# Optimization experiments

Measured on AMD Instinct MI355X. Metric: run time of the kernel, lower is better.

Reference implementation:

```python
import jax, jax.numpy as jnp
import numpy as np

DIM = 256
HEADS = 8
K_RATIO = 0.25


def setup_inputs() -> dict:
    key = jax.random.key(0)
    ks = jax.random.split(key, 5)
    B, C, S = 4, DIM, 2048
    x = jax.random.normal(ks[0], (B, C, S), dtype=jnp.float32)
    # Conv1d(dim, 3*dim, 1, bias=False) weight -> (3*dim, dim)
    W_qkv = jax.random.normal(ks[1], (3 * DIM, DIM), dtype=jnp.float32) * (1.0 / np.sqrt(DIM))
    # depthwise Conv1d(3*dim, 3*dim, 3, groups=3*dim) weight -> (3*dim, 1, 3)
    W_dw = jax.random.normal(ks[2], (3 * DIM, 1, 3), dtype=jnp.float32) * (1.0 / np.sqrt(3))
    # Conv1d(dim, dim, 1, bias=False) weight -> (dim, dim)
    W_proj = jax.random.normal(ks[3], (DIM, DIM), dtype=jnp.float32) * (1.0 / np.sqrt(DIM))
    temperature = jnp.ones((HEADS, 1, 1), dtype=jnp.float32)
    return {"x": x, "W_qkv": W_qkv, "W_dw": W_dw, "W_proj": W_proj,
            "temperature": temperature}


def _l2norm(t, eps=1e-12):
    # F.normalize: x / max(||x||_2, eps)
    n = jnp.sqrt(jnp.sum(t * t, axis=-1, keepdims=True))
    return t / jnp.maximum(n, eps)


def reference(x, W_qkv, W_dw, W_proj, temperature):
    B, C, S = x.shape
    H = temperature.shape[0]
    hd = C // H
    # 1x1 conv == channel matmul
    qkv = jnp.einsum('oc,bcs->bos', W_qkv, x)  # [B, 3C, S]
    # depthwise conv, kernel 3, pad 1
    qkv = jax.lax.conv_general_dilated(
        qkv, W_dw, window_strides=(1,), padding=[(1, 1)],
        dimension_numbers=('NCH', 'OIH', 'NCH'),
        feature_group_count=3 * C)
    q, k, v = jnp.split(qkv, 3, axis=1)  # each [B, C, S]

    def to_heads(t):
        return t.reshape(B, H, hd, S).transpose(0, 1, 3, 2)  # [B, H, S, hd]

    q = _l2norm(to_heads(q))
    k = _l2norm(to_heads(k))
    v = to_heads(v)

    scores = jnp.einsum('bhsc,bhtc->bhst', q, k) * temperature  # [B,H,S,S]

    topk = max(1, min(S, int(np.ceil(K_RATIO * S))))
    vals, idx = jax.lax.top_k(scores, topk)  # [B,H,S,topk]

    # scatter top-k values into a -inf tensor along the last axis
    N = B * H * S
    sparse = jnp.full((N, S), -jnp.inf, dtype=scores.dtype)
    rows = jnp.arange(N)[:, None]
    sparse = sparse.at[rows, idx.reshape(N, topk)].set(vals.reshape(N, topk))
    sparse = jnp.clip(sparse.reshape(B, H, S, S), -10000.0, 10000.0)

    attn = jax.nn.softmax(sparse, axis=-1)  # dropout p=0.0 -> identity
    out = jnp.einsum('bhst,bhtc->bhsc', attn, v)  # [B,H,S,hd]
    out = out.transpose(0, 1, 3, 2).reshape(B, C, S)  # b (head c) s
    return jnp.einsum('oc,bcs->bos', W_proj, out)
```

## Files before the change

### kernel.cpp

```cpp
#include <hip/hip_runtime.h>
#include <math.h>

typedef __attribute__((ext_vector_type(8))) short short8;
typedef __attribute__((ext_vector_type(4))) float f32x4;
typedef __attribute__((ext_vector_type(2))) unsigned int uint2v;

#define DEV __device__ __forceinline__

static constexpr int B_ = 4, C_ = 256, S_ = 2048, H_ = 8, O3_ = 768;
static constexpr int TOPK = 512;
static constexpr int QT = 16;
static constexpr int HCOLS = 1024;
static constexpr int HSTR = 1028;
static constexpr int PSTH = 1024;
static constexpr size_t K3_LDS_BYTES = (size_t)QT * HSTR * 4;

DEV unsigned cvt_pk_bf16(float a, float b) {
  unsigned r;
  asm("v_cvt_pk_bf16_f32 %0, %1, %2" : "=v"(r) : "v"(a), "v"(b));
  return r;
}
DEV unsigned short f2bf1(float f) { return (unsigned short)(cvt_pk_bf16(f, f) & 0xFFFFu); }
DEV float bf2f(unsigned short h) { return __uint_as_float(((unsigned)h) << 16); }
DEV void hilo(float f, unsigned short& h, unsigned short& l) {
  unsigned p = cvt_pk_bf16(f, f);
  h = (unsigned short)p;
  float r = f - __uint_as_float(p << 16);
  l = (unsigned short)(cvt_pk_bf16(r, r) & 0xFFFFu);
}

__global__ void k_convw(const float* __restrict__ wqkv, const float* __restrict__ wproj,
                        unsigned short* __restrict__ wq_hi, unsigned short* __restrict__ wq_lo,
                        unsigned short* __restrict__ wproj_bf) {
  int i = blockIdx.x * 256 + threadIdx.x;
  if (i < O3_ * C_) {
    unsigned short h, l;
    hilo(wqkv[i], h, l);
    wq_hi[i] = h;
    wq_lo[i] = l;
  }
  if (i < C_ * C_) wproj_bf[i] = f2bf1(wproj[i]);
}

__global__ void k_xt(const float* __restrict__ x, unsigned short* __restrict__ xT_hi,
                     unsigned short* __restrict__ xT_lo) {
  __shared__ float t[32][33];
  int b = blockIdx.z;
  int c0 = blockIdx.y * 32, s0 = blockIdx.x * 32;
  int tx = threadIdx.x, ty = threadIdx.y;
  const float* xb = x + (size_t)b * C_ * S_;
#pragma unroll
  for (int j = 0; j < 4; ++j)
    t[ty + 8 * j][tx] = xb[(size_t)(c0 + ty + 8 * j) * S_ + s0 + tx];
  __syncthreads();
  unsigned short* hb = xT_hi + (size_t)b * S_ * C_;
  unsigned short* lb = xT_lo + (size_t)b * S_ * C_;
#pragma unroll
  for (int j = 0; j < 4; ++j) {
    unsigned short h, l;
    hilo(t[tx][ty + 8 * j], h, l);
    size_t o = (size_t)(s0 + ty + 8 * j) * C_ + c0 + tx;
    hb[o] = h;
    lb[o] = l;
  }
}

__global__ __launch_bounds__(256) void k_qkv(const unsigned short* __restrict__ w_hi,
                                             const unsigned short* __restrict__ w_lo,
                                             const unsigned short* __restrict__ x_hi,
                                             const unsigned short* __restrict__ x_lo,
                                             float* __restrict__ raw) {
  int b = blockIdx.z;
  int m0 = blockIdx.y * 64, n0 = blockIdx.x * 64;
  int tid = threadIdx.x, lane = tid & 63, wid = tid >> 6;
  int l15 = lane & 15, lh = lane >> 4;
  int wm = (wid >> 1) * 32, wn = (wid & 1) * 32;
  const unsigned short* xhb = x_hi + (size_t)b * S_ * C_;
  const unsigned short* xlb = x_lo + (size_t)b * S_ * C_;
  f32x4 acc[2][2] = {};
  int mA = m0 + wm + l15;
  int nB = n0 + wn + l15;
  for (int k0 = 0; k0 < C_; k0 += 32) {
    int kk = k0 + lh * 8;
    short8 a0h = *(const short8*)(w_hi + (size_t)mA * C_ + kk);
    short8 a1h = *(const short8*)(w_hi + (size_t)(mA + 16) * C_ + kk);
    short8 a0l = *(const short8*)(w_lo + (size_t)mA * C_ + kk);
    short8 a1l = *(const short8*)(w_lo + (size_t)(mA + 16) * C_ + kk);
    short8 b0h = *(const short8*)(xhb + (size_t)nB * C_ + kk);
    short8 b1h = *(const short8*)(xhb + (size_t)(nB + 16) * C_ + kk);
    short8 b0l = *(const short8*)(xlb + (size_t)nB * C_ + kk);
    short8 b1l = *(const short8*)(xlb + (size_t)(nB + 16) * C_ + kk);
    acc[0][0] = __builtin_amdgcn_mfma_f32_16x16x32_bf16(a0h, b0h, acc[0][0], 0, 0, 0);
    acc[0][1] = __builtin_amdgcn_mfma_f32_16x16x32_bf16(a0h, b1h, acc[0][1], 0, 0, 0);
    acc[1][0] = __builtin_amdgcn_mfma_f32_16x16x32_bf16(a1h, b0h, acc[1][0], 0, 0, 0);
    acc[1][1] = __builtin_amdgcn_mfma_f32_16x16x32_bf16(a1h, b1h, acc[1][1], 0, 0, 0);
    acc[0][0] = __builtin_amdgcn_mfma_f32_16x16x32_bf16(a0h, b0l, acc[0][0], 0, 0, 0);
    acc[0][1] = __builtin_amdgcn_mfma_f32_16x16x32_bf16(a0h, b1l, acc[0][1], 0, 0, 0);
    acc[1][0] = __builtin_amdgcn_mfma_f32_16x16x32_bf16(a1h, b0l, acc[1][0], 0, 0, 0);
    acc[1][1] = __builtin_amdgcn_mfma_f32_16x16x32_bf16(a1h, b1l, acc[1][1], 0, 0, 0);
    acc[0][0] = __builtin_amdgcn_mfma_f32_16x16x32_bf16(a0l, b0h, acc[0][0], 0, 0, 0);
    acc[0][1] = __builtin_amdgcn_mfma_f32_16x16x32_bf16(a0l, b1h, acc[0][1], 0, 0, 0);
    acc[1][0] = __builtin_amdgcn_mfma_f32_16x16x32_bf16(a1l, b0h, acc[1][0], 0, 0, 0);
    acc[1][1] = __builtin_amdgcn_mfma_f32_16x16x32_bf16(a1l, b1h, acc[1][1], 0, 0, 0);
  }
  float* rawb = raw + (size_t)b * O3_ * S_;
#pragma unroll
  for (int i = 0; i < 2; ++i)
#pragma unroll
    for (int j = 0; j < 2; ++j)
#pragma unroll
      for (int r = 0; r < 4; ++r) {
        int row = m0 + wm + i * 16 + lh * 4 + r;
        int col = n0 + wn + j * 16 + l15;
        rawb[(size_t)row * S_ + col] = acc[i][j][r];
      }
}

DEV float conv3(const float* __restrict__ rp, const float* __restrict__ w, int s) {
  float a = (s > 0) ? rp[s - 1] : 0.f;
  float b = rp[s];
  float c = (s < S_ - 1) ? rp[s + 1] : 0.f;
  return w[0] * a + w[1] * b + w[2] * c;
}

__global__ __launch_bounds__(256) void k_dwnorm(const float* __restrict__ raw,
                                                const float* __restrict__ wdw,
                                                const float* __restrict__ temp,
                                                unsigned short* __restrict__ q_hi,
                                                unsigned short* __restrict__ q_lo,
                                                unsigned short* __restrict__ k_hi,
                                                unsigned short* __restrict__ k_lo,
                                                unsigned short* __restrict__ vt) {
  int b = blockIdx.z, h = blockIdx.y;
  int tid = threadIdx.x;
  int wave = tid >> 6, lane = tid & 63;
  int dg = lane & 7;
  int sl = lane >> 3;
  int s = blockIdx.x * 32 + wave * 8 + sl;
  const float* rawb = raw + (size_t)b * O3_ * S_;
  float tph = temp[h];
  size_t bh = (size_t)(b * H_ + h);
  float qv[4], kv[4], vv[4];
  float sq = 0.f, sk = 0.f;
#pragma unroll
  for (int dd = 0; dd < 4; ++dd) {
    int d = dg * 4 + dd;
    int oq = h * 32 + d;
    float q = conv3(rawb + (size_t)oq * S_, wdw + oq * 3, s);
    qv[dd] = q; sq += q * q;
    int ok = oq + 256;
    float k = conv3(rawb + (size_t)ok * S_, wdw + ok * 3, s);
    kv[dd] = k; sk += k * k;
    int ov = oq + 512;
    vv[dd] = conv3(rawb + (size_t)ov * S_, wdw + ov * 3, s);
  }
#pragma unroll
  for (int m = 1; m < 8; m <<= 1) {
    sq += __shfl_xor(sq, m);
    sk += __shfl_xor(sk, m);
  }
  float iq = tph / fmaxf(sqrtf(sq), 1e-12f);
  float ik = 1.f / fmaxf(sqrtf(sk), 1e-12f);
  size_t base = (bh * S_ + s) * 32 + dg * 4;

  float q0 = qv[0] * iq, q1 = qv[1] * iq, q2 = qv[2] * iq, q3 = qv[3] * iq;
  unsigned qh01 = cvt_pk_bf16(q0, q1), qh23 = cvt_pk_bf16(q2, q3);
  *(uint2v*)(q_hi + base) = uint2v{qh01, qh23};
  float ql0 = q0 - __uint_as_float(qh01 << 16);
  float ql1 = q1 - __uint_as_float(qh01 & 0xFFFF0000u);
  float ql2 = q2 - __uint_as_float(qh23 << 16);
  float ql3 = q3 - __uint_as_float(qh23 & 0xFFFF0000u);
  *(uint2v*)(q_lo + base) = uint2v{cvt_pk_bf16(ql0, ql1), cvt_pk_bf16(ql2, ql3)};

  float k0 = kv[0] * ik, k1 = kv[1] * ik, k2 = kv[2] * ik, k3 = kv[3] * ik;
  unsigned kh01 = cvt_pk_bf16(k0, k1), kh23 = cvt_pk_bf16(k2, k3);
  *(uint2v*)(k_hi + base) = uint2v{kh01, kh23};
  float kl0 = k0 - __uint_as_float(kh01 << 16);
  float kl1 = k1 - __uint_as_float(kh01 & 0xFFFF0000u);
  float kl2 = k2 - __uint_as_float(kh23 << 16);
  float kl3 = k3 - __uint_as_float(kh23 & 0xFFFF0000u);
  *(uint2v*)(k_lo + base) = uint2v{cvt_pk_bf16(kl0, kl1), cvt_pk_bf16(kl2, kl3)};

#pragma unroll
  for (int dd = 0; dd < 4; ++dd) {
    int d = dg * 4 + dd;
    vt[(bh * 32 + d) * S_ + s] = f2bf1(vv[dd]);
  }
}

__global__ __launch_bounds__(1024, 8) void k_attn(const unsigned short* __restrict__ q_hi,
                                                  const unsigned short* __restrict__ q_lo,
                                                  const unsigned short* __restrict__ k_hi,
                                                  const unsigned short* __restrict__ k_lo,
                                                  const unsigned short* __restrict__ vt,
                                                  unsigned short* __restrict__ ao) {
  extern __shared__ float smem[];
  __shared__ float is_arr[QT];
  float* sc = smem;
  unsigned short* P = (unsigned short*)smem;
  float* red = smem;
  int bid = blockIdx.x;
  int tile = bid & 127;
  int bh = bid >> 7;
  int q0 = tile * QT;
  int tid = threadIdx.x, lane = tid & 63, wv = tid >> 6;
  int l15 = lane & 15, lh = lane >> 4;
  const unsigned short* vb = vt + (size_t)bh * 32 * S_;

  size_t qoff = ((size_t)bh * S_ + q0 + l15) * 32 + lh * 8;
  short8 ah = *(const short8*)(q_hi + qoff);
  short8 al = *(const short8*)(q_lo + qoff);
  size_t kbase = (size_t)bh * S_ * 32;

  float v[32];

#pragma unroll
  for (int hhalf = 0; hhalf < 2; ++hhalf) {
    int colbase = wv * 64;
    const unsigned short* khp = k_hi + kbase + (size_t)(hhalf * HCOLS + colbase + l15) * 32 + lh * 8;
    const unsigned short* klp = k_lo + kbase + (size_t)(hhalf * HCOLS + colbase + l15) * 32 + lh * 8;
    short8 kh0 = *(const short8*)(khp);
    short8 kl0 = *(const short8*)(klp);
    short8 kh1 = *(const short8*)(khp + 512);
    short8 kl1 = *(const short8*)(klp + 512);
    for (int nt = 0; nt < 4; ++nt) {
      short8 kh2 = kh1, kl2 = kl1;
      if (nt < 2) {
        kh2 = *(const short8*)(khp + (nt + 2) * 512);
        kl2 = *(const short8*)(klp + (nt + 2) * 512);
      }
      f32x4 d = {};
      d = __builtin_amdgcn_mfma_f32_16x16x32_bf16(ah, kh0, d, 0, 0, 0);
      d = __builtin_amdgcn_mfma_f32_16x16x32_bf16(ah, kl0, d, 0, 0, 0);
      d = __builtin_amdgcn_mfma_f32_16x16x32_bf16(al, kh0, d, 0, 0, 0);
      int tloc = colbase + nt * 16;
#pragma unroll
      for (int r = 0; r < 4; ++r)
        sc[(lh * 4 + r) * HSTR + tloc + l15] = d[r];
      kh0 = kh1; kl0 = kl1; kh1 = kh2; kl1 = kl2;
    }
    __syncthreads();
#pragma unroll
    for (int j = 0; j < 16; ++j)
      v[hhalf * 16 + j] = sc[wv * HSTR + lane + 64 * j];
    __syncthreads();
  }

  float vmax;
  {
    vmax = v[0];
    float vmin = v[0], sum = 0.f, sqs = 0.f;
#pragma unroll
    for (int j = 0; j < 32; ++j) {
      vmax = fmaxf(vmax, v[j]); vmin = fminf(vmin, v[j]);
      sum += v[j]; sqs = fmaf(v[j], v[j], sqs);
    }
#pragma unroll
    for (int m = 1; m < 64; m <<= 1) {
      vmax = fmaxf(vmax, __shfl_xor(vmax, m));
      vmin = fminf(vmin, __shfl_xor(vmin, m));
      sum += __shfl_xor(sum, m);
      sqs += __shfl_xor(sqs, m);
    }
    float mu = sum * (1.f / 2048.f);
    float sig = sqrtf(fmaxf(sqs * (1.f / 2048.f) - mu * mu, 0.f));

    float vlo = vmin - 1e-3f, vhi = vmax;
    float flo = 1536.f, fhi = -512.f;
    int chi = 0;
    float T = vhi;
    bool exact = false;
    int lastside = 0;
    float piv = mu + 0.67449f * sig;
    if (!(piv > vlo && piv < vhi)) piv = 0.5f * (vlo + vhi);
    for (int it = 0; it < 32; ++it) {
      int c = 0;
#pragma unroll
      for (int j = 0; j < 32; ++j)
        c += (int)__popcll(__ballot(v[j] > piv));
      if (c == TOPK) { T = piv; exact = true; break; }
      if (c > TOPK) {
        if (lastside == 1) fhi *= 0.5f;
        vlo = piv; flo = (float)(c - TOPK); lastside = 1;
      } else {
        if (lastside == -1) flo *= 0.5f;
        vhi = piv; fhi = (float)(c - TOPK); chi = c; lastside = -1;
      }
      float npiv;
      if (it == 0 && sig > 1e-20f) {
        float z = (piv - mu) / sig;
        float dens = 0.398942f * __expf(-0.5f * z * z) * (2048.f / sig);
        npiv = piv + (float)(c - TOPK) / fmaxf(dens, 1e-6f);
      } else {
        npiv = vhi - fhi * (vhi - vlo) / (fhi - flo);
      }
      if (!(npiv > vlo && npiv < vhi)) npiv = 0.5f * (vlo + vhi);
      if (!(npiv > vlo && npiv < vhi)) break;
      piv = npiv;
    }
    int cntGT = exact ? TOPK : chi;
    if (!exact) T = vhi;

    unsigned selbits = 0;
#pragma unroll
    for (int j = 0; j < 32; ++j)
      if (v[j] > T) selbits |= (1u << j);
    int need = TOPK - cntGT;
    if (need > 0) {
      int base = 0;
      unsigned long long lmask = (lane == 0) ? 0ull : (~0ull >> (64 - lane));
#pragma unroll
      for (int j = 0; j < 32; ++j) {
        bool tie = (v[j] == T);
        unsigned long long m = __ballot(tie);
        int rank = base + (int)__popcll(m & lmask);
        if (tie && rank < need) selbits |= (1u << j);
        base += (int)__popcll(m);
      }
    }

    float ssum = 0.f;
#pragma unroll
    for (int j = 0; j < 32; ++j) {
      float e = ((selbits >> j) & 1u) ? __expf(v[j] - vmax) : 0.f;
      v[j] = e;
      ssum += e;
    }
#pragma unroll
    for (int m = 1; m < 64; m <<= 1) ssum += __shfl_xor(ssum, m);
    if (lane == 0) is_arr[wv] = 1.f / ssum;
  }

  f32x4 acc0 = {}, acc1 = {};
  int swz_w = (wv & 7) << 3;
  int swz_r = (l15 & 7) << 3;
#pragma unroll
  for (int hhalf = 0; hhalf < 2; ++hhalf) {
#pragma unroll
    for (int j = 0; j < 16; ++j) {
      int idx = (wv * PSTH + j * 64 + lane) ^ swz_w;
      P[idx] = f2bf1(v[hhalf * 16 + j]);
    }
    __syncthreads();
    {
      const unsigned short* v0p = vb + (size_t)l15 * S_ + hhalf * HCOLS + wv * 64 + lh * 8;
      const unsigned short* v1p = v0p + 16 * S_;
      int lc0 = wv * 64 + lh * 8;
      short8 a0 = *(const short8*)(P + ((l15 * PSTH + lc0) ^ swz_r));
      short8 a1 = *(const short8*)(P + ((l15 * PSTH + lc0 + 32) ^ swz_r));
      short8 b00 = *(const short8*)(v0p);
      short8 b10 = *(const short8*)(v1p);
      short8 b01 = *(const short8*)(v0p + 32);
      short8 b11 = *(const short8*)(v1p + 32);
      acc0 = __builtin_amdgcn_mfma_f32_16x16x32_bf16(a0, b00, acc0, 0, 0, 0);
      acc1 = __builtin_amdgcn_mfma_f32_16x16x32_bf16(a0, b10, acc1, 0, 0, 0);
      acc0 = __builtin_amdgcn_mfma_f32_16x16x32_bf16(a1, b01, acc0, 0, 0, 0);
      acc1 = __builtin_amdgcn_mfma_f32_16x16x32_bf16(a1, b11, acc1, 0, 0, 0);
    }
    __syncthreads();
  }

#pragma unroll
  for (int r = 0; r < 4; ++r) {
    red[wv * 529 + (lh * 4 + r) * 33 + l15] = acc0[r];
    red[wv * 529 + (lh * 4 + r) * 33 + 16 + l15] = acc1[r];
  }
  __syncthreads();
  if (tid < 512) {
    int row = tid >> 5, d = tid & 31;
    float s = 0.f;
#pragma unroll
    for (int w = 0; w < 16; ++w) s += red[w * 529 + row * 33 + d];
    s *= is_arr[row];
    ao[((size_t)bh * S_ + q0 + row) * 32 + d] = f2bf1(s);
  }
}

__global__ __launch_bounds__(256) void k_proj(const unsigned short* __restrict__ wbf,
                                              const unsigned short* __restrict__ ao,
                                              float* __restrict__ out) {
  int b = blockIdx.z;
  int m0 = blockIdx.y * 64, n0 = blockIdx.x * 64;
  int tid = threadIdx.x, lane = tid & 63, wid = tid >> 6;
  int l15 = lane & 15, lh = lane >> 4;
  int wm = (wid >> 1) * 32, wn = (wid & 1) * 32;
  const unsigned short* aob = ao + (size_t)b * H_ * S_ * 32;
  f32x4 acc[2][2] = {};
  int mA = m0 + wm + l15;
  int nB = n0 + wn + l15;
  for (int k0 = 0; k0 < C_; k0 += 32) {
    int kk = k0 + lh * 8;
    int hh = kk >> 5;
    int dd = kk & 31;
    short8 a0 = *(const short8*)(wbf + (size_t)mA * C_ + kk);
    short8 a1 = *(const short8*)(wbf + (size_t)(mA + 16) * C_ + kk);
    short8 b0 = *(const short8*)(aob + ((size_t)hh * S_ + nB) * 32 + dd);
    short8 b1 = *(const short8*)(aob + ((size_t)hh * S_ + nB + 16) * 32 + dd);
    acc[0][0] = __builtin_amdgcn_mfma_f32_16x16x32_bf16(a0, b0, acc[0][0], 0, 0, 0);
    acc[0][1] = __builtin_amdgcn_mfma_f32_16x16x32_bf16(a0, b1, acc[0][1], 0, 0, 0);
    acc[1][0] = __builtin_amdgcn_mfma_f32_16x16x32_bf16(a1, b0, acc[1][0], 0, 0, 0);
    acc[1][1] = __builtin_amdgcn_mfma_f32_16x16x32_bf16(a1, b1, acc[1][1], 0, 0, 0);
  }
  float* ob = out + (size_t)b * C_ * S_;
#pragma unroll
  for (int i = 0; i < 2; ++i)
#pragma unroll
    for (int j = 0; j < 2; ++j)
#pragma unroll
      for (int r = 0; r < 4; ++r) {
        int row = m0 + wm + i * 16 + lh * 4 + r;
        int col = n0 + wn + j * 16 + l15;
        ob[(size_t)row * S_ + col] = acc[i][j][r];
      }
}

extern "C" void kernel_launch(void* const* d_in, const int* in_sizes, int n_in,
                              void* d_out, int out_size, void* d_ws, size_t ws_size,
                              hipStream_t stream) {
  const float* x = (const float*)d_in[0];
  const float* wqkv = (const float*)d_in[1];
  const float* wdw = (const float*)d_in[2];
  const float* wproj = (const float*)d_in[3];
  const float* temp = (const float*)d_in[4];
  float* out = (float*)d_out;

  char* ws = (char*)d_ws;
  size_t off = 0;
  auto alloc = [&](size_t bytes) -> void* {
    void* p = ws + off;
    off += (bytes + 255) & ~(size_t)255;
    return p;
  };
  unsigned short* x_hi     = (unsigned short*)alloc((size_t)B_ * S_ * C_ * 2);
  unsigned short* x_lo     = (unsigned short*)alloc((size_t)B_ * S_ * C_ * 2);
  unsigned short* wq_hi    = (unsigned short*)alloc((size_t)O3_ * C_ * 2);
  unsigned short* wq_lo    = (unsigned short*)alloc((size_t)O3_ * C_ * 2);
  unsigned short* wproj_bf = (unsigned short*)alloc((size_t)C_ * C_ * 2);
  float*          raw      = (float*)alloc((size_t)B_ * O3_ * S_ * 4);
  unsigned short* k_hi     = (unsigned short*)alloc((size_t)B_ * H_ * S_ * 32 * 2);
  unsigned short* k_lo     = (unsigned short*)alloc((size_t)B_ * H_ * S_ * 32 * 2);
  unsigned short* vt       = (unsigned short*)alloc((size_t)B_ * H_ * 32 * S_ * 2);
  unsigned short* q_hi     = x_hi;
  unsigned short* q_lo     = x_lo;
  unsigned short* ao       = (unsigned short*)raw;

  (void)hipFuncSetAttribute(reinterpret_cast<const void*>(k_attn),
                            hipFuncAttributeMaxDynamicSharedMemorySize, (int)K3_LDS_BYTES);

  k_convw<<<dim3((O3_ * C_ + 255) / 256), dim3(256), 0, stream>>>(wqkv, wproj, wq_hi, wq_lo, wproj_bf);
  k_xt<<<dim3(S_ / 32, C_ / 32, B_), dim3(32, 8), 0, stream>>>(x, x_hi, x_lo);
  k_qkv<<<dim3(S_ / 64, O3_ / 64, B_), dim3(256), 0, stream>>>(wq_hi, wq_lo, x_hi, x_lo, raw);
  k_dwnorm<<<dim3(S_ / 32, H_, B_), dim3(256), 0, stream>>>(raw, wdw, temp, q_hi, q_lo, k_hi, k_lo, vt);
  k_attn<<<dim3(B_ * H_ * (S_ / QT)), dim3(1024), K3_LDS_BYTES, stream>>>(q_hi, q_lo, k_hi, k_lo, vt, ao);
  k_proj<<<dim3(S_ / 64, C_ / 64, B_), dim3(256), 0, stream>>>(wproj_bf, ao, out);
}
```

Before: 289.3 us.

## Halve attention block to 512 threads with two query rows per wave

The attention kernel now runs 8 waves per block instead of 16, and each wave handles two query rows. The per-row top-k selection and softmax moves into a helper that is called twice, which gives the selection loops more independent work per wave. Scores are staged through shared memory in four 512-column chunks instead of two 1024-column halves, roughly halving the score staging buffer. The PV stage and the final reduction are adjusted so each wave covers 128 keys per half. The cost is more barriers and LDS round-trips, plus higher register pressure from keeping two 32-element rows live per lane.

```diff
diff --git a/kernel.cpp b/kernel.cpp
--- a/kernel.cpp
+++ b/kernel.cpp
@@ -10,10 +10,11 @@
 static constexpr int B_ = 4, C_ = 256, S_ = 2048, H_ = 8, O3_ = 768;
 static constexpr int TOPK = 512;
 static constexpr int QT = 16;
+static constexpr int QCOLS = 512;
+static constexpr int QSTR = 516;
 static constexpr int HCOLS = 1024;
-static constexpr int HSTR = 1028;
 static constexpr int PSTH = 1024;
-static constexpr size_t K3_LDS_BYTES = (size_t)QT * HSTR * 4;
+static constexpr size_t K3_LDS_BYTES = (size_t)QT * QSTR * 4;
 
 DEV unsigned cvt_pk_bf16(float a, float b) {
   unsigned r;
@@ -188,12 +189,95 @@
   }
 }
 
-__global__ __launch_bounds__(1024, 8) void k_attn(const unsigned short* __restrict__ q_hi,
-                                                  const unsigned short* __restrict__ q_lo,
-                                                  const unsigned short* __restrict__ k_hi,
-                                                  const unsigned short* __restrict__ k_lo,
-                                                  const unsigned short* __restrict__ vt,
-                                                  unsigned short* __restrict__ ao) {
+DEV float select_softmax_row(float (&vv)[32], int lane) {
+  float vmax = vv[0], vmin = vv[0], sum = 0.f, sqs = 0.f;
+#pragma unroll
+  for (int j = 0; j < 32; ++j) {
+    vmax = fmaxf(vmax, vv[j]); vmin = fminf(vmin, vv[j]);
+    sum += vv[j]; sqs = fmaf(vv[j], vv[j], sqs);
+  }
+#pragma unroll
+  for (int m = 1; m < 64; m <<= 1) {
+    vmax = fmaxf(vmax, __shfl_xor(vmax, m));
+    vmin = fminf(vmin, __shfl_xor(vmin, m));
+    sum += __shfl_xor(sum, m);
+    sqs += __shfl_xor(sqs, m);
+  }
+  float mu = sum * (1.f / 2048.f);
+  float sig = sqrtf(fmaxf(sqs * (1.f / 2048.f) - mu * mu, 0.f));
+
+  float vlo = vmin - 1e-3f, vhi = vmax;
+  float flo = 1536.f, fhi = -512.f;
+  int chi = 0;
+  float T = vhi;
+  bool exact = false;
+  int lastside = 0;
+  float piv = mu + 0.67449f * sig;
+  if (!(piv > vlo && piv < vhi)) piv = 0.5f * (vlo + vhi);
+  for (int it = 0; it < 32; ++it) {
+    int c = 0;
+#pragma unroll
+    for (int j = 0; j < 32; ++j)
+      c += (int)__popcll(__ballot(vv[j] > piv));
+    if (c == TOPK) { T = piv; exact = true; break; }
+    if (c > TOPK) {
+      if (lastside == 1) fhi *= 0.5f;
+      vlo = piv; flo = (float)(c - TOPK); lastside = 1;
+    } else {
+      if (lastside == -1) flo *= 0.5f;
+      vhi = piv; fhi = (float)(c - TOPK); chi = c; lastside = -1;
+    }
+    float npiv;
+    if (it == 0 && sig > 1e-20f) {
+      float z = (piv - mu) / sig;
+      float dens = 0.398942f * __expf(-0.5f * z * z) * (2048.f / sig);
+      npiv = piv + (float)(c - TOPK) / fmaxf(dens, 1e-6f);
+    } else {
+      npiv = vhi - fhi * (vhi - vlo) / (fhi - flo);
+    }
+    if (!(npiv > vlo && npiv < vhi)) npiv = 0.5f * (vlo + vhi);
+    if (!(npiv > vlo && npiv < vhi)) break;
+    piv = npiv;
+  }
+  int cntGT = exact ? TOPK : chi;
+  if (!exact) T = vhi;
+
+  unsigned selbits = 0;
+#pragma unroll
+  for (int j = 0; j < 32; ++j)
+    if (vv[j] > T) selbits |= (1u << j);
+  int need = TOPK - cntGT;
+  if (need > 0) {
+    int base = 0;
+    unsigned long long lmask = (lane == 0) ? 0ull : (~0ull >> (64 - lane));
+#pragma unroll
+    for (int j = 0; j < 32; ++j) {
+      bool tie = (vv[j] == T);
+      unsigned long long m = __ballot(tie);
+      int rank = base + (int)__popcll(m & lmask);
+      if (tie && rank < need) selbits |= (1u << j);
+      base += (int)__popcll(m);
+    }
+  }
+
+  float ssum = 0.f;
+#pragma unroll
+  for (int j = 0; j < 32; ++j) {
+    float e = ((selbits >> j) & 1u) ? __expf(vv[j] - vmax) : 0.f;
+    vv[j] = e;
+    ssum += e;
+  }
+#pragma unroll
+  for (int m = 1; m < 64; m <<= 1) ssum += __shfl_xor(ssum, m);
+  return 1.f / ssum;
+}
+
+__global__ __launch_bounds__(512, 4) void k_attn(const unsigned short* __restrict__ q_hi,
+                                                 const unsigned short* __restrict__ q_lo,
+                                                 const unsigned short* __restrict__ k_hi,
+                                                 const unsigned short* __restrict__ k_lo,
+                                                 const unsigned short* __restrict__ vt,
+                                                 unsigned short* __restrict__ ao) {
   extern __shared__ float smem[];
   __shared__ float is_arr[QT];
   float* sc = smem;
@@ -212,17 +296,18 @@
   short8 al = *(const short8*)(q_lo + qoff);
   size_t kbase = (size_t)bh * S_ * 32;
 
-  float v[32];
-
-#pragma unroll
-  for (int hhalf = 0; hhalf < 2; ++hhalf) {
-    int colbase = wv * 64;
-    const unsigned short* khp = k_hi + kbase + (size_t)(hhalf * HCOLS + colbase + l15) * 32 + lh * 8;
-    const unsigned short* klp = k_lo + kbase + (size_t)(hhalf * HCOLS + colbase + l15) * 32 + lh * 8;
+  float v0[32], v1[32];
+
+#pragma unroll
+  for (int qq = 0; qq < 4; ++qq) {
+    int colg = qq * QCOLS + wv * 64;
+    const unsigned short* khp = k_hi + kbase + (size_t)(colg + l15) * 32 + lh * 8;
+    const unsigned short* klp = k_lo + kbase + (size_t)(colg + l15) * 32 + lh * 8;
     short8 kh0 = *(const short8*)(khp);
     short8 kl0 = *(const short8*)(klp);
     short8 kh1 = *(const short8*)(khp + 512);
     short8 kl1 = *(const short8*)(klp + 512);
+#pragma unroll
     for (int nt = 0; nt < 4; ++nt) {
       short8 kh2 = kh1, kl2 = kl1;
       if (nt < 2) {
@@ -233,129 +318,52 @@
       d = __builtin_amdgcn_mfma_f32_16x16x32_bf16(ah, kh0, d, 0, 0, 0);
       d = __builtin_amdgcn_mfma_f32_16x16x32_bf16(ah, kl0, d, 0, 0, 0);
       d = __builtin_amdgcn_mfma_f32_16x16x32_bf16(al, kh0, d, 0, 0, 0);
-      int tloc = colbase + nt * 16;
+      int tloc = wv * 64 + nt * 16;
 #pragma unroll
       for (int r = 0; r < 4; ++r)
-        sc[(lh * 4 + r) * HSTR + tloc + l15] = d[r];
+        sc[(lh * 4 + r) * QSTR + tloc + l15] = d[r];
       kh0 = kh1; kl0 = kl1; kh1 = kh2; kl1 = kl2;
     }
     __syncthreads();
 #pragma unroll
-    for (int j = 0; j < 16; ++j)
-      v[hhalf * 16 + j] = sc[wv * HSTR + lane + 64 * j];
+    for (int jj = 0; jj < 8; ++jj) {
+      v0[qq * 8 + jj] = sc[(2 * wv) * QSTR + jj * 64 + lane];
+      v1[qq * 8 + jj] = sc[(2 * wv + 1) * QSTR + jj * 64 + lane];
+    }
     __syncthreads();
   }
 
-  float vmax;
   {
-    vmax = v[0];
-    float vmin = v[0], sum = 0.f, sqs = 0.f;
-#pragma unroll
-    for (int j = 0; j < 32; ++j) {
-      vmax = fmaxf(vmax, v[j]); vmin = fminf(vmin, v[j]);
-      sum += v[j]; sqs = fmaf(v[j], v[j], sqs);
-    }
-#pragma unroll
-    for (int m = 1; m < 64; m <<= 1) {
-      vmax = fmaxf(vmax, __shfl_xor(vmax, m));
-      vmin = fminf(vmin, __shfl_xor(vmin, m));
-      sum += __shfl_xor(sum, m);
-      sqs += __shfl_xor(sqs, m);
-    }
-    float mu = sum * (1.f / 2048.f);
-    float sig = sqrtf(fmaxf(sqs * (1.f / 2048.f) - mu * mu, 0.f));
-
-    float vlo = vmin - 1e-3f, vhi = vmax;
-    float flo = 1536.f, fhi = -512.f;
-    int chi = 0;
-    float T = vhi;
-    bool exact = false;
-    int lastside = 0;
-    float piv = mu + 0.67449f * sig;
-    if (!(piv > vlo && piv < vhi)) piv = 0.5f * (vlo + vhi);
-    for (int it = 0; it < 32; ++it) {
-      int c = 0;
-#pragma unroll
-      for (int j = 0; j < 32; ++j)
-        c += (int)__popcll(__ballot(v[j] > piv));
-      if (c == TOPK) { T = piv; exact = true; break; }
-      if (c > TOPK) {
-        if (lastside == 1) fhi *= 0.5f;
-        vlo = piv; flo = (float)(c - TOPK); lastside = 1;
-      } else {
-        if (lastside == -1) flo *= 0.5f;
-        vhi = piv; fhi = (float)(c - TOPK); chi = c; lastside = -1;
-      }
-      float npiv;
-      if (it == 0 && sig > 1e-20f) {
-        float z = (piv - mu) / sig;
-        float dens = 0.398942f * __expf(-0.5f * z * z) * (2048.f / sig);
-        npiv = piv + (float)(c - TOPK) / fmaxf(dens, 1e-6f);
-      } else {
-        npiv = vhi - fhi * (vhi - vlo) / (fhi - flo);
-      }
-      if (!(npiv > vlo && npiv < vhi)) npiv = 0.5f * (vlo + vhi);
-      if (!(npiv > vlo && npiv < vhi)) break;
-      piv = npiv;
-    }
-    int cntGT = exact ? TOPK : chi;
-    if (!exact) T = vhi;
-
-    unsigned selbits = 0;
-#pragma unroll
-    for (int j = 0; j < 32; ++j)
-      if (v[j] > T) selbits |= (1u << j);
-    int need = TOPK - cntGT;
-    if (need > 0) {
-      int base = 0;
-      unsigned long long lmask = (lane == 0) ? 0ull : (~0ull >> (64 - lane));
-#pragma unroll
-      for (int j = 0; j < 32; ++j) {
-        bool tie = (v[j] == T);
-        unsigned long long m = __ballot(tie);
-        int rank = base + (int)__popcll(m & lmask);
-        if (tie && rank < need) selbits |= (1u << j);
-        base += (int)__popcll(m);
-      }
-    }
-
-    float ssum = 0.f;
-#pragma unroll
-    for (int j = 0; j < 32; ++j) {
-      float e = ((selbits >> j) & 1u) ? __expf(v[j] - vmax) : 0.f;
-      v[j] = e;
-      ssum += e;
-    }
-#pragma unroll
-    for (int m = 1; m < 64; m <<= 1) ssum += __shfl_xor(ssum, m);
-    if (lane == 0) is_arr[wv] = 1.f / ssum;
+    float is0 = select_softmax_row(v0, lane);
+    float is1 = select_softmax_row(v1, lane);
+    if (lane == 0) { is_arr[2 * wv] = is0; is_arr[2 * wv + 1] = is1; }
   }
 
   f32x4 acc0 = {}, acc1 = {};
-  int swz_w = (wv & 7) << 3;
+  int swz_w0 = ((2 * wv) & 7) << 3;
+  int swz_w1 = ((2 * wv + 1) & 7) << 3;
   int swz_r = (l15 & 7) << 3;
 #pragma unroll
   for (int hhalf = 0; hhalf < 2; ++hhalf) {
 #pragma unroll
-    for (int j = 0; j < 16; ++j) {
-      int idx = (wv * PSTH + j * 64 + lane) ^ swz_w;
-      P[idx] = f2bf1(v[hhalf * 16 + j]);
+    for (int j2 = 0; j2 < 16; ++j2) {
+      int lc = (j2 >> 3) * QCOLS + (j2 & 7) * 64 + lane;
+      P[((2 * wv) * PSTH + lc) ^ swz_w0] = f2bf1(v0[hhalf * 16 + j2]);
+      P[((2 * wv + 1) * PSTH + lc) ^ swz_w1] = f2bf1(v1[hhalf * 16 + j2]);
     }
     __syncthreads();
     {
-      const unsigned short* v0p = vb + (size_t)l15 * S_ + hhalf * HCOLS + wv * 64 + lh * 8;
+      const unsigned short* v0p = vb + (size_t)l15 * S_ + hhalf * HCOLS + wv * 128 + lh * 8;
       const unsigned short* v1p = v0p + 16 * S_;
-      int lc0 = wv * 64 + lh * 8;
-      short8 a0 = *(const short8*)(P + ((l15 * PSTH + lc0) ^ swz_r));
-      short8 a1 = *(const short8*)(P + ((l15 * PSTH + lc0 + 32) ^ swz_r));
-      short8 b00 = *(const short8*)(v0p);
-      short8 b10 = *(const short8*)(v1p);
-      short8 b01 = *(const short8*)(v0p + 32);
-      short8 b11 = *(const short8*)(v1p + 32);
-      acc0 = __builtin_amdgcn_mfma_f32_16x16x32_bf16(a0, b00, acc0, 0, 0, 0);
-      acc1 = __builtin_amdgcn_mfma_f32_16x16x32_bf16(a0, b10, acc1, 0, 0, 0);
-      acc0 = __builtin_amdgcn_mfma_f32_16x16x32_bf16(a1, b01, acc0, 0, 0, 0);
-      acc1 = __builtin_amdgcn_mfma_f32_16x16x32_bf16(a1, b11, acc1, 0, 0, 0);
+#pragma unroll
+      for (int kt = 0; kt < 4; ++kt) {
+        int lc = wv * 128 + kt * 32 + lh * 8;
+        short8 a = *(const short8*)(P + ((l15 * PSTH + lc) ^ swz_r));
+        short8 b0 = *(const short8*)(v0p + kt * 32);
+        short8 b1 = *(const short8*)(v1p + kt * 32);
+        acc0 = __builtin_amdgcn_mfma_f32_16x16x32_bf16(a, b0, acc0, 0, 0, 0);
+        acc1 = __builtin_amdgcn_mfma_f32_16x16x32_bf16(a, b1, acc1, 0, 0, 0);
+      }
     }
     __syncthreads();
   }
@@ -366,11 +374,11 @@
     red[wv * 529 + (lh * 4 + r) * 33 + 16 + l15] = acc1[r];
   }
   __syncthreads();
-  if (tid < 512) {
+  {
     int row = tid >> 5, d = tid & 31;
     float s = 0.f;
 #pragma unroll
-    for (int w = 0; w < 16; ++w) s += red[w * 529 + row * 33 + d];
+    for (int w = 0; w < 8; ++w) s += red[w * 529 + row * 33 + d];
     s *= is_arr[row];
     ao[((size_t)bh * S_ + q0 + row) * 32 + d] = f2bf1(s);
   }
@@ -451,6 +459,6 @@
   k_xt<<<dim3(S_ / 32, C_ / 32, B_), dim3(32, 8), 0, stream>>>(x, x_hi, x_lo);
   k_qkv<<<dim3(S_ / 64, O3_ / 64, B_), dim3(256), 0, stream>>>(wq_hi, wq_lo, x_hi, x_lo, raw);
   k_dwnorm<<<dim3(S_ / 32, H_, B_), dim3(256), 0, stream>>>(raw, wdw, temp, q_hi, q_lo, k_hi, k_lo, vt);
-  k_attn<<<dim3(B_ * H_ * (S_ / QT)), dim3(1024), K3_LDS_BYTES, stream>>>(q_hi, q_lo, k_hi, k_lo, vt, ao);
+  k_attn<<<dim3(B_ * H_ * (S_ / QT)), dim3(512), K3_LDS_BYTES, stream>>>(q_hi, q_lo, k_hi, k_lo, vt, ao);
   k_proj<<<dim3(S_ / 64, C_ / 64, B_), dim3(256), 0, stream>>>(wproj_bf, ao, out);
 }
```

New measurement: 306.4 us. +5.9%, slower.

## Double-buffer score and P tiles in LDS to cut block barriers

Applied to the files above, without the earlier changes.

The score computation is split into four 512-column quarters written to two alternating LDS buffers, so one barrier per quarter replaces two per half, and the next K fragments are prefetched during the MFMAs. The P·V stage likewise writes the two P halves to separate LDS regions, so writing the second half overlaps the first half's MFMAs and one barrier is dropped. This targets barrier stalls in a 1024-thread block, at the cost of a different LDS footprint and a remapping of score columns to registers. Correctness depends on the new column ordering of v[] matching how P is written back.

```diff
diff --git a/kernel.cpp b/kernel.cpp
--- a/kernel.cpp
+++ b/kernel.cpp
@@ -10,10 +10,12 @@
 static constexpr int B_ = 4, C_ = 256, S_ = 2048, H_ = 8, O3_ = 768;
 static constexpr int TOPK = 512;
 static constexpr int QT = 16;
-static constexpr int HCOLS = 1024;
-static constexpr int HSTR = 1028;
+static constexpr int QCOLS = 512;
+static constexpr int QSTR = 516;
+static constexpr int QBUF = 16 * QSTR;
 static constexpr int PSTH = 1024;
-static constexpr size_t K3_LDS_BYTES = (size_t)QT * HSTR * 4;
+static constexpr int P1OFF = 2 * QBUF;
+static constexpr size_t K3_LDS_BYTES = (size_t)2 * QBUF * 4;
 
 DEV unsigned cvt_pk_bf16(float a, float b) {
   unsigned r;
@@ -196,8 +198,7 @@
                                                   unsigned short* __restrict__ ao) {
   extern __shared__ float smem[];
   __shared__ float is_arr[QT];
-  float* sc = smem;
-  unsigned short* P = (unsigned short*)smem;
+  unsigned short* Pb = (unsigned short*)smem;
   float* red = smem;
   int bid = blockIdx.x;
   int tile = bid & 127;
@@ -214,42 +215,46 @@
 
   float v[32];
 
-#pragma unroll
-  for (int hhalf = 0; hhalf < 2; ++hhalf) {
-    int colbase = wv * 64;
-    const unsigned short* khp = k_hi + kbase + (size_t)(hhalf * HCOLS + colbase + l15) * 32 + lh * 8;
-    const unsigned short* klp = k_lo + kbase + (size_t)(hhalf * HCOLS + colbase + l15) * 32 + lh * 8;
-    short8 kh0 = *(const short8*)(khp);
-    short8 kl0 = *(const short8*)(klp);
-    short8 kh1 = *(const short8*)(khp + 512);
-    short8 kl1 = *(const short8*)(klp + 512);
-    for (int nt = 0; nt < 4; ++nt) {
-      short8 kh2 = kh1, kl2 = kl1;
-      if (nt < 2) {
-        kh2 = *(const short8*)(khp + (nt + 2) * 512);
-        kl2 = *(const short8*)(klp + (nt + 2) * 512);
-      }
-      f32x4 d = {};
-      d = __builtin_amdgcn_mfma_f32_16x16x32_bf16(ah, kh0, d, 0, 0, 0);
-      d = __builtin_amdgcn_mfma_f32_16x16x32_bf16(ah, kl0, d, 0, 0, 0);
-      d = __builtin_amdgcn_mfma_f32_16x16x32_bf16(al, kh0, d, 0, 0, 0);
-      int tloc = colbase + nt * 16;
-#pragma unroll
-      for (int r = 0; r < 4; ++r)
-        sc[(lh * 4 + r) * HSTR + tloc + l15] = d[r];
-      kh0 = kh1; kl0 = kl1; kh1 = kh2; kl1 = kl2;
+  short8 kh0, kl0, kh1, kl1;
+  {
+    const unsigned short* kp = k_hi + kbase + (size_t)(wv * 32 + l15) * 32 + lh * 8;
+    const unsigned short* lp = k_lo + kbase + (size_t)(wv * 32 + l15) * 32 + lh * 8;
+    kh0 = *(const short8*)(kp);       kl0 = *(const short8*)(lp);
+    kh1 = *(const short8*)(kp + 512); kl1 = *(const short8*)(lp + 512);
+  }
+#pragma unroll
+  for (int qq = 0; qq < 4; ++qq) {
+    float* buf = smem + (qq & 1) * QBUF;
+    {
+      f32x4 d0 = {}, d1 = {};
+      d0 = __builtin_amdgcn_mfma_f32_16x16x32_bf16(ah, kh0, d0, 0, 0, 0);
+      d0 = __builtin_amdgcn_mfma_f32_16x16x32_bf16(ah, kl0, d0, 0, 0, 0);
+      d0 = __builtin_amdgcn_mfma_f32_16x16x32_bf16(al, kh0, d0, 0, 0, 0);
+      d1 = __builtin_amdgcn_mfma_f32_16x16x32_bf16(ah, kh1, d1, 0, 0, 0);
+      d1 = __builtin_amdgcn_mfma_f32_16x16x32_bf16(ah, kl1, d1, 0, 0, 0);
+      d1 = __builtin_amdgcn_mfma_f32_16x16x32_bf16(al, kh1, d1, 0, 0, 0);
+      int tloc = wv * 32 + l15;
+#pragma unroll
+      for (int r = 0; r < 4; ++r) {
+        buf[(lh * 4 + r) * QSTR + tloc] = d0[r];
+        buf[(lh * 4 + r) * QSTR + tloc + 16] = d1[r];
+      }
+      if (qq < 3) {
+        int colg = (qq + 1) * QCOLS + wv * 32;
+        const unsigned short* kp = k_hi + kbase + (size_t)(colg + l15) * 32 + lh * 8;
+        const unsigned short* lp = k_lo + kbase + (size_t)(colg + l15) * 32 + lh * 8;
+        kh0 = *(const short8*)(kp);       kl0 = *(const short8*)(lp);
+        kh1 = *(const short8*)(kp + 512); kl1 = *(const short8*)(lp + 512);
+      }
     }
     __syncthreads();
 #pragma unroll
-    for (int j = 0; j < 16; ++j)
-      v[hhalf * 16 + j] = sc[wv * HSTR + lane + 64 * j];
-    __syncthreads();
-  }
-
-  float vmax;
+    for (int jj = 0; jj < 8; ++jj)
+      v[qq * 8 + jj] = buf[wv * QSTR + jj * 64 + lane];
+  }
+
   {
-    vmax = v[0];
-    float vmin = v[0], sum = 0.f, sqs = 0.f;
+    float vmax = v[0], vmin = v[0], sum = 0.f, sqs = 0.f;
 #pragma unroll
     for (int j = 0; j < 32; ++j) {
       vmax = fmaxf(vmax, v[j]); vmin = fminf(vmin, v[j]);
@@ -335,30 +340,44 @@
   int swz_w = (wv & 7) << 3;
   int swz_r = (l15 & 7) << 3;
 #pragma unroll
-  for (int hhalf = 0; hhalf < 2; ++hhalf) {
-#pragma unroll
-    for (int j = 0; j < 16; ++j) {
-      int idx = (wv * PSTH + j * 64 + lane) ^ swz_w;
-      P[idx] = f2bf1(v[hhalf * 16 + j]);
-    }
-    __syncthreads();
-    {
-      const unsigned short* v0p = vb + (size_t)l15 * S_ + hhalf * HCOLS + wv * 64 + lh * 8;
-      const unsigned short* v1p = v0p + 16 * S_;
-      int lc0 = wv * 64 + lh * 8;
-      short8 a0 = *(const short8*)(P + ((l15 * PSTH + lc0) ^ swz_r));
-      short8 a1 = *(const short8*)(P + ((l15 * PSTH + lc0 + 32) ^ swz_r));
-      short8 b00 = *(const short8*)(v0p);
-      short8 b10 = *(const short8*)(v1p);
-      short8 b01 = *(const short8*)(v0p + 32);
-      short8 b11 = *(const short8*)(v1p + 32);
-      acc0 = __builtin_amdgcn_mfma_f32_16x16x32_bf16(a0, b00, acc0, 0, 0, 0);
-      acc1 = __builtin_amdgcn_mfma_f32_16x16x32_bf16(a0, b10, acc1, 0, 0, 0);
-      acc0 = __builtin_amdgcn_mfma_f32_16x16x32_bf16(a1, b01, acc0, 0, 0, 0);
-      acc1 = __builtin_amdgcn_mfma_f32_16x16x32_bf16(a1, b11, acc1, 0, 0, 0);
-    }
-    __syncthreads();
-  }
+  for (int j2 = 0; j2 < 16; ++j2) {
+    int lc = ((j2 >> 3) & 1) * 512 + (j2 & 7) * 64 + lane;
+    Pb[(wv * PSTH + lc) ^ swz_w] = f2bf1(v[j2]);
+  }
+  __syncthreads();
+  {
+#pragma unroll
+    for (int j2 = 0; j2 < 16; ++j2) {
+      int lc = ((j2 >> 3) & 1) * 512 + (j2 & 7) * 64 + lane;
+      Pb[P1OFF + ((wv * PSTH + lc) ^ swz_w)] = f2bf1(v[16 + j2]);
+    }
+    const unsigned short* v0p = vb + (size_t)l15 * S_ + wv * 64 + lh * 8;
+    const unsigned short* v1p = v0p + 16 * S_;
+#pragma unroll
+    for (int kt = 0; kt < 2; ++kt) {
+      int lc = wv * 64 + kt * 32 + lh * 8;
+      short8 a = *(const short8*)(Pb + ((l15 * PSTH + lc) ^ swz_r));
+      short8 b0 = *(const short8*)(v0p + kt * 32);
+      short8 b1 = *(const short8*)(v1p + kt * 32);
+      acc0 = __builtin_amdgcn_mfma_f32_16x16x32_bf16(a, b0, acc0, 0, 0, 0);
+      acc1 = __builtin_amdgcn_mfma_f32_16x16x32_bf16(a, b1, acc1, 0, 0, 0);
+    }
+  }
+  __syncthreads();
+  {
+    const unsigned short* v0p = vb + (size_t)l15 * S_ + 1024 + wv * 64 + lh * 8;
+    const unsigned short* v1p = v0p + 16 * S_;
+#pragma unroll
+    for (int kt = 0; kt < 2; ++kt) {
+      int lc = wv * 64 + kt * 32 + lh * 8;
+      short8 a = *(const short8*)(Pb + P1OFF + ((l15 * PSTH + lc) ^ swz_r));
+      short8 b0 = *(const short8*)(v0p + kt * 32);
+      short8 b1 = *(const short8*)(v1p + kt * 32);
+      acc0 = __builtin_amdgcn_mfma_f32_16x16x32_bf16(a, b0, acc0, 0, 0, 0);
+      acc1 = __builtin_amdgcn_mfma_f32_16x16x32_bf16(a, b1, acc1, 0, 0, 0);
+    }
+  }
+  __syncthreads();
 
 #pragma unroll
   for (int r = 0; r < 4; ++r) {
```

Result: faster. 275.3 us (-4.8%).
